# Kernel optimization log

Hardware: AMD Instinct MI355X
Metric: run time of the kernel (lower is better)

## Reference

```python
import jax, jax.numpy as jnp
import numpy as np

GAMMAS = (0.01, 0.1, 1.0, 10.0, 100.0)
FOCAL_GAMMA = 2.0
SMOOTH = 0.1
TASK_W = (0.4, 0.3, 0.3)
A_RECON, A_ORTH, A_ADV = 1.0, 0.1, 0.1
NUM_DOMAINS = 4
NUM_LABELS1 = 4


def focal_smooth(logits, targets, maskf):
    # FocalLoss.forward with smoothing > 0, masked mean
    n_classes = logits.shape[1]
    log_p = jax.nn.log_softmax(logits, axis=1)
    p = jnp.exp(log_p)
    onehot = jax.nn.one_hot(targets, n_classes, dtype=logits.dtype)
    smooth = onehot * (1.0 - SMOOTH) + SMOOTH / n_classes
    ce = -(smooth * log_p).sum(axis=1)
    pt = jnp.take_along_axis(p, targets[:, None], axis=1)[:, 0]
    loss = ce * (1.0 - pt) ** FOCAL_GAMMA
    return (loss * maskf).sum() / jnp.maximum(maskf.sum(), 1.0)


def ce_masked(logits, targets, maskf):
    log_p = jax.nn.log_softmax(logits, axis=1)
    nll = -jnp.take_along_axis(log_p, targets[:, None], axis=1)[:, 0]
    return (nll * maskf).sum() / jnp.maximum(maskf.sum(), 1.0)


def cond_mmd(feats, domains, labels, maskf):
    # Global pairwise sq-distance matrix; multi-gamma RBF kernels summed.
    sq = (feats ** 2).sum(axis=-1)                      # (B,)
    Dmat = sq[:, None] + sq[None, :] - 2.0 * feats @ feats.T  # (B,B)
    Ksum = jnp.zeros_like(Dmat)
    for g in GAMMAS:
        Ksum = Ksum + jnp.exp(-g * Dmat)
    loss = jnp.asarray(0.0, feats.dtype)
    count = jnp.asarray(0.0, feats.dtype)
    for lab in range(NUM_LABELS1):
        lm = (labels == lab).astype(feats.dtype) * maskf
        for d1 in range(NUM_DOMAINS):
            m1 = lm * (domains == d1).astype(feats.dtype)
            n1 = m1.sum()
            Km1 = Ksum @ m1
            for d2 in range(d1 + 1, NUM_DOMAINS):
                m2 = lm * (domains == d2).astype(feats.dtype)
                n2 = m2.sum()
                valid = (n1 > 1) & (n2 > 1)
                term = (m1 @ Km1) / jnp.maximum(n1, 1.0) ** 2 \
                     + (m2 @ (Ksum @ m2)) / jnp.maximum(n2, 1.0) ** 2 \
                     - 2.0 * (m2 @ Km1) / jnp.maximum(n1 * n2, 1.0)
                loss = loss + jnp.where(valid, term, 0.0)
                count = count + valid.astype(feats.dtype)
    return loss / jnp.maximum(count, 1.0)


def hsic(c, s):
    n = c.shape[0]
    c = c / jnp.maximum(jnp.linalg.norm(c, axis=-1, keepdims=True), 1e-12)
    s = s / jnp.maximum(jnp.linalg.norm(s, axis=-1, keepdims=True), 1e-12)
    K = c @ c.T
    L = s @ s.T
    Kc = K - K.mean(axis=0, keepdims=True) - K.mean(axis=1, keepdims=True) + K.mean()
    Lc = L - L.mean(axis=0, keepdims=True) - L.mean(axis=1, keepdims=True) + L.mean()
    return (Kc * Lc).sum() / (n - 1) ** 2


def setup_inputs() -> dict:
    key = jax.random.key(0)
    ks = jax.random.split(key, 20)
    B, D, H = 4096, 256, 768
    inp = {
        'logits1': jax.random.normal(ks[0], (B, 4), jnp.float32),
        'labels1': jax.random.randint(ks[1], (B,), 0, 4),
        'logits2': jax.random.normal(ks[2], (B, 6), jnp.float32),
        'labels2': jax.random.randint(ks[3], (B,), 0, 6),
        'logits3': jax.random.normal(ks[4], (B, 3), jnp.float32),
        'labels3': jax.random.randint(ks[5], (B,), 0, 3),
        'c_v': jax.random.normal(ks[6], (B, D), jnp.float32),
        's_v': jax.random.normal(ks[7], (B, D), jnp.float32),
        'c_t': jax.random.normal(ks[8], (B, D), jnp.float32),
        's_t': jax.random.normal(ks[9], (B, D), jnp.float32),
        'v_sv': jax.random.normal(ks[10], (B, NUM_DOMAINS), jnp.float32),
        'v_st': jax.random.normal(ks[11], (B, NUM_DOMAINS), jnp.float32),
        'domain_labels': jax.random.randint(ks[12], (B,), 0, NUM_DOMAINS),
        'mask': jnp.ones((B,), dtype=bool),
        'h_img_recon': jax.random.normal(ks[13], (B, H), jnp.float32),
        'h_img_orig': jax.random.normal(ks[14], (B, H), jnp.float32),
        'h_txt_recon': jax.random.normal(ks[15], (B, H), jnp.float32),
        'h_txt_orig': jax.random.normal(ks[16], (B, H), jnp.float32),
    }
    return inp


def reference(logits1, labels1, logits2, labels2, logits3, labels3,
              c_v, s_v, c_t, s_t, v_sv, v_st, domain_labels, mask,
              h_img_recon, h_img_orig, h_txt_recon, h_txt_orig):
    maskf = mask.astype(jnp.float32)
    total = jnp.asarray(0.0, jnp.float32)
    # classification (focal + label smoothing), per-task weighted
    total = total + TASK_W[0] * focal_smooth(logits1, labels1, maskf)
    total = total + TASK_W[1] * focal_smooth(logits2, labels2, maskf)
    total = total + TASK_W[2] * focal_smooth(logits3, labels3, maskf)
    # adversarial: CE on spurious domain logits + conditional MMD on causal feats
    l_adv_s = ce_masked(v_sv, domain_labels, maskf) + ce_masked(v_st, domain_labels, maskf)
    l_adv_c = cond_mmd(c_v, domain_labels, labels1, maskf) \
            + cond_mmd(c_t, domain_labels, labels1, maskf)
    total = total + A_ADV * (l_adv_s + l_adv_c)
    # orthogonality (HSIC), on unmasked features as in source
    l_orth = hsic(c_v, s_v) + hsic(c_t, s_t)
    total = total + A_ORTH * l_orth
    # reconstruction MSE
    l_recon = jnp.mean((h_img_recon - h_img_orig) ** 2) + jnp.mean((h_txt_recon - h_txt_orig) ** 2)
    total = total + A_RECON * l_recon
    return total
```

## Files before the change

### kernel.cpp

```cpp
#include <hip/hip_runtime.h>
#include <hip/hip_bf16.h>


typedef short bf16x8 __attribute__((ext_vector_type(8)));
typedef float f32x4 __attribute__((ext_vector_type(4)));
typedef unsigned long long u64;
typedef unsigned int u32;

static constexpr int D = 256;
static constexpr int H = 768;
static constexpr int NG = 16;
static constexpr float FX32 = 4294967296.f;
static constexpr float IFX32 = 2.3283064365386963e-10f;

__device__ inline void gAddFx(u64* p, float v) {
  long long q = (long long)llroundf(v * FX32);
  atomicAdd(p, (u64)q);
}
__device__ inline float fxToF(u64 v) { return (float)(long long)v * IFX32; }

__device__ inline float focal_n(const float* x, int n, int tgt,
                                float s_over_n, float oms) {
  float mx = x[0];
  for (int c = 1; c < n; ++c) mx = fmaxf(mx, x[c]);
  float se = 0.f, sx = 0.f;
  for (int c = 0; c < n; ++c) { se += __expf(x[c] - mx); sx += x[c]; }
  float logZ = mx + __logf(se);
  float ce = logZ - oms * x[tgt] - s_over_n * sx;
  float pt = __expf(x[tgt] - logZ);
  float om = 1.f - pt;
  return ce * om * om;
}

extern "C" __global__ __launch_bounds__(256) void k_pre(
    const void* __restrict__ mask, const int* __restrict__ y1,
    const int* __restrict__ dom,
    const float* __restrict__ l1, const float* __restrict__ l2,
    const float* __restrict__ l3, const int* __restrict__ y2,
    const int* __restrict__ y3,
    const float* __restrict__ vsv, const float* __restrict__ vst,
    const float* __restrict__ cv, const float* __restrict__ sv,
    const float* __restrict__ ct, const float* __restrict__ st,
    const float* __restrict__ ir, const float* __restrict__ io,
    const float* __restrict__ trc, const float* __restrict__ to,
    u64* SA, u64* GCU, u64* U64,
    int* gid, float* sq, float* inv, unsigned short* bf, u32* CNTB,
    int B, int N4, int NA, int NB) {
  __shared__ u32 sh3[3];
  __shared__ u32 cnt[17];
  __shared__ int redi[4];
  __shared__ float redf[4];
  int bid = blockIdx.x;
  int t = threadIdx.x;

  if (bid < NA) {
    if (t < 3) sh3[t] = 0;
    if (t < 17) cnt[t] = 0;
    __syncthreads();
    u32 a = 0, b2 = 0, cd = 0;
    if (t * 16 + 15 < B) {
      uint4 wv = ((const uint4*)mask)[t];
      u32 ws[4] = {wv.x, wv.y, wv.z, wv.w};
      #pragma unroll
      for (int j = 0; j < 4; ++j) {
        a |= ws[j] & 0xffu; b2 |= ws[j] & 0xff00u; cd |= ws[j] & 0xffff0000u;
      }
    }
    if (a) atomicOr(&sh3[0], 1u);
    if (b2) atomicOr(&sh3[1], 1u);
    if (cd) atomicOr(&sh3[2], 1u);
    __syncthreads();
    int mode;
    if ((sh3[1] | sh3[2]) == 0) mode = 0;
    else if (sh3[0] == 0 && sh3[1] == 0) mode = 1;
    else mode = 2;
    int r = bid * 256 + t;
    int mi = 0;
    float s[5] = {0.f, 0.f, 0.f, 0.f, 0.f};
    if (r < B) {
      if (mode == 0)      mi = ((const int*)mask)[r] ? 1 : 0;
      else if (mode == 1) mi = (((const float*)mask)[r] != 0.f) ? 1 : 0;
      else                mi = ((const unsigned char*)mask)[r] ? 1 : 0;
      int g = -1;
      if (mi) { g = y1[r] * 4 + dom[r]; atomicAdd(&cnt[g], 1u); }
      else atomicAdd(&cnt[16], 1u);
      gid[r] = g;
      if (mi) {
        float x[6];
        for (int c = 0; c < 4; ++c) x[c] = l1[r * 4 + c];
        s[0] = focal_n(x, 4, y1[r], 0.1f / 4.f, 0.9f);
        for (int c = 0; c < 6; ++c) x[c] = l2[r * 6 + c];
        s[1] = focal_n(x, 6, y2[r], 0.1f / 6.f, 0.9f);
        for (int c = 0; c < 3; ++c) x[c] = l3[r * 3 + c];
        s[2] = focal_n(x, 3, y3[r], 0.1f / 3.f, 0.9f);
        int d = dom[r];
        for (int c = 0; c < 4; ++c) x[c] = vsv[r * 4 + c];
        {
          float mx = fmaxf(fmaxf(x[0], x[1]), fmaxf(x[2], x[3]));
          float se = __expf(x[0]-mx)+__expf(x[1]-mx)+__expf(x[2]-mx)+__expf(x[3]-mx);
          s[3] = mx + __logf(se) - x[d];
        }
        for (int c = 0; c < 4; ++c) x[c] = vst[r * 4 + c];
        {
          float mx = fmaxf(fmaxf(x[0], x[1]), fmaxf(x[2], x[3]));
          float se = __expf(x[0]-mx)+__expf(x[1]-mx)+__expf(x[2]-mx)+__expf(x[3]-mx);
          s[4] = mx + __logf(se) - x[d];
        }
      }
    }
    int v = mi;
    #pragma unroll
    for (int o = 32; o > 0; o >>= 1) v += __shfl_down(v, o);
    if ((t & 63) == 0) redi[t >> 6] = v;
    __syncthreads();
    if (t == 0) atomicAdd(&SA[5], (u64)(redi[0] + redi[1] + redi[2] + redi[3]));
    if (t < NG && cnt[t]) atomicAdd(&GCU[t], (u64)cnt[t]);
    if (t < 17) CNTB[bid * 17 + t] = cnt[t];
    for (int k = 0; k < 5; ++k) {
      float x = s[k];
      #pragma unroll
      for (int o = 32; o > 0; o >>= 1) x += __shfl_down(x, o);
      __syncthreads();
      if ((t & 63) == 0) redf[t >> 6] = x;
      __syncthreads();
      if (t == 0) gAddFx(&SA[k], redf[0] + redf[1] + redf[2] + redf[3]);
    }
  } else if (bid < NA + NB) {
    int b = bid - NA;
    int f = b >> 6;
    int rb = b & 63;
    const float* p = (f == 0) ? cv : (f == 1) ? sv : (f == 2) ? ct : st;
    int w = t >> 6, L = t & 63;
    float up0 = 0.f, up1 = 0.f, up2 = 0.f, up3 = 0.f;
    for (int k = 0; k < 16; ++k) {
      int r = rb * 64 + w * 16 + k;
      float4 v = ((const float4*)(p + (size_t)r * D))[L];
      float ss = v.x * v.x + v.y * v.y + v.z * v.z + v.w * v.w;
      #pragma unroll
      for (int o = 32; o > 0; o >>= 1) ss += __shfl_down(ss, o);
      ss = __shfl(ss, 0);
      float iv = 1.f / fmaxf(sqrtf(ss), 1e-12f);
      if ((f & 1) == 0) {
        int fi = f >> 1;
        alignas(8) __hip_bfloat16 hb[4];
        hb[0] = __float2bfloat16(v.x); hb[1] = __float2bfloat16(v.y);
        hb[2] = __float2bfloat16(v.z); hb[3] = __float2bfloat16(v.w);
        *(uint2*)(bf + ((size_t)fi * B + r) * D + L * 4) = *(uint2*)hb;
        if (L == 0) sq[fi * B + r] = ss;
      }
      if (L == 0) inv[f * B + r] = iv;
      up0 += v.x * iv; up1 += v.y * iv; up2 += v.z * iv; up3 += v.w * iv;
    }
    u64* Uf = U64 + f * D + 4 * L;
    gAddFx(Uf + 0, up0); gAddFx(Uf + 1, up1);
    gAddFx(Uf + 2, up2); gAddFx(Uf + 3, up3);
  } else {
    int cidx = bid - (NA + NB);
    int j = cidx >> 8;
    int cb = cidx & 255;
    const float4* A  = (const float4*)(j ? trc : ir);
    const float4* Bp = (const float4*)(j ? to : io);
    float acc = 0.f;
    for (int idx = cb * 256 + t; idx < N4; idx += 256 * 256) {
      float4 a = A[idx], b = Bp[idx];
      float dx = a.x-b.x, dy = a.y-b.y, dz = a.z-b.z, dw = a.w-b.w;
      acc += dx*dx + dy*dy + dz*dz + dw*dw;
    }
    #pragma unroll
    for (int o = 32; o > 0; o >>= 1) acc += __shfl_down(acc, o);
    if ((t & 63) == 0) redf[t >> 6] = acc;
    __syncthreads();
    if (t == 0) gAddFx(&SA[6 + j], redf[0] + redf[1] + redf[2] + redf[3]);
  }
}

extern "C" __global__ __launch_bounds__(256) void k_mid(
    const u32* __restrict__ CNTB, const int* __restrict__ gid,
    const float* __restrict__ sq,
    const float* __restrict__ cv, const float* __restrict__ sv,
    const float* __restrict__ ct, const float* __restrict__ st,
    const float* __restrict__ inv,
    int* __restrict__ perm, float* __restrict__ sqp, int* __restrict__ OFF,
    unsigned short* __restrict__ bnT, int B, int NA) {
  __shared__ float ld[64 * 65];
  __shared__ u32 cbs[17], tots[17], wcnt[4][17];
  __shared__ u32 base[18];
  int b = blockIdx.x, t = threadIdx.x;

  if (b < NA) {
    if (t < 68) ((u32*)wcnt)[t] = 0;
    if (t < 17) {
      u32 cb = 0, tot = 0;
      for (int b2 = 0; b2 < NA; ++b2) {
        u32 c = CNTB[b2 * 17 + t];
        cb += (b2 < b) ? c : 0u;
        tot += c;
      }
      cbs[t] = cb; tots[t] = tot;
    }
    int r = b * 256 + t;
    int g = 16;
    if (r < B) { int gg = gid[r]; g = (gg < 0) ? 16 : gg; }
    __syncthreads();
    if (t == 0) {
      u32 s = 0;
      for (int g2 = 0; g2 < 17; ++g2) { base[g2] = s; s += tots[g2]; }
      base[17] = s;
    }
    u64 msk = ~0ull;
    #pragma unroll
    for (int bit = 0; bit < 5; ++bit) {
      int bv = (g >> bit) & 1;
      u64 bl = __ballot(bv);
      msk &= bv ? bl : ~bl;
    }
    int lane = t & 63, w = t >> 6;
    int rwave = __popcll(msk & ((1ull << lane) - 1ull));
    if (rwave == 0) wcnt[w][g] = (u32)__popcll(msk);
    __syncthreads();
    if (r < B) {
      int rank = rwave;
      for (int w2 = 0; w2 < 4; ++w2) if (w2 < w) rank += (int)wcnt[w2][g];
      int pos = (int)(base[g] + cbs[g]) + rank;
      perm[pos] = r;
      sqp[pos] = sq[r];
      sqp[B + pos] = sq[B + r];
    }
    if (b == 0 && t < 18) OFF[t] = (int)base[t];
  } else {
    int TPF = (B >> 6) * 4;
    int tb = b - NA;
    int fm = tb / TPF, tile = tb - fm * TPF;
    int it = tile >> 2, at = tile & 3;
    const float* src = (fm == 0) ? cv : (fm == 1) ? sv : (fm == 2) ? ct : st;
    const float* ivf = inv + (size_t)fm * B;
    int i0 = it * 64, a0 = at * 64;
    for (int e = t; e < 1024; e += 256) {
      int i = e >> 4, c4 = e & 15;
      float4 v = ((const float4*)(src + (size_t)(i0 + i) * D))[at * 16 + c4];
      float ivv = ivf[i0 + i];
      ld[i * 65 + c4 * 4 + 0] = v.x * ivv;
      ld[i * 65 + c4 * 4 + 1] = v.y * ivv;
      ld[i * 65 + c4 * 4 + 2] = v.z * ivv;
      ld[i * 65 + c4 * 4 + 3] = v.w * ivv;
    }
    __syncthreads();
    unsigned short* dst = bnT + (size_t)fm * D * B;
    for (int e = t; e < 512; e += 256) {
      int a = e >> 3, ic = e & 7;
      alignas(16) unsigned short h[8];
      #pragma unroll
      for (int j = 0; j < 8; ++j) {
        __hip_bfloat16 hb = __float2bfloat16(ld[(ic * 8 + j) * 65 + a]);
        h[j] = *(unsigned short*)&hb;
      }
      *(uint4*)(dst + (size_t)(a0 + a) * B + i0 + ic * 8) = *(uint4*)h;
    }
  }
}

extern "C" __global__ __launch_bounds__(256) void k_big(
    const unsigned short* __restrict__ bf, const float* __restrict__ sqp,
    const int* __restrict__ perm, const int* __restrict__ OFF,
    const unsigned short* __restrict__ bnT, float* __restrict__ Mf32,
    u64* GSP, int B) {
  __shared__ __align__(16) char smem[17536];
  unsigned short* Ab = (unsigned short*)smem;
  unsigned short* Bb = (unsigned short*)(smem + 8192);
  int bid = blockIdx.x;
  int tid = threadIdx.x;
  int w = tid >> 6, L = tid & 63, m = L & 15, q = L >> 4;
  int r0 = tid >> 3, ck = tid & 7;
  int swz = (ck ^ (r0 & 7)) * 8;
  int ar = w * 16 + m;

  if (bid < 64) {
    int half = bid & 1, bb = (bid >> 1) & 3, ab = (bid >> 3) & 3, p = (bid >> 5) & 1;
    const unsigned short* Abase = bnT + (size_t)(2 * p) * D * B;
    const unsigned short* Bbase = bnT + (size_t)(2 * p + 1) * D * B;
    size_t kof = (size_t)half * (B >> 1) + ck * 8;
    const uint4* gA0 = (const uint4*)(Abase + (size_t)(ab * 64 + r0) * B + kof);
    const uint4* gA1 = (const uint4*)(Abase + (size_t)(ab * 64 + r0 + 32) * B + kof);
    const uint4* gB0 = (const uint4*)(Bbase + (size_t)(bb * 64 + r0) * B + kof);
    const uint4* gB1 = (const uint4*)(Bbase + (size_t)(bb * 64 + r0 + 32) * B + kof);
    uint4* dA0 = (uint4*)&Ab[r0 * 64 + swz];
    uint4* dA1 = (uint4*)&Ab[(r0 + 32) * 64 + swz];
    uint4* dB0 = (uint4*)&Bb[r0 * 64 + swz];
    uint4* dB1 = (uint4*)&Bb[(r0 + 32) * 64 + swz];
    f32x4 acc[4] = {{0.f,0.f,0.f,0.f},{0.f,0.f,0.f,0.f},
                    {0.f,0.f,0.f,0.f},{0.f,0.f,0.f,0.f}};
    int nh = B >> 7;
    for (int hq = 0; hq < nh; ++hq) {
      *dA0 = gA0[hq * 8]; *dA1 = gA1[hq * 8];
      *dB0 = gB0[hq * 8]; *dB1 = gB1[hq * 8];
      __syncthreads();
      #pragma unroll
      for (int kk = 0; kk < 2; ++kk) {
        bf16x8 aF = *(const bf16x8*)&Ab[ar * 64 + (((kk * 4 + q) ^ (ar & 7)) * 8)];
        #pragma unroll
        for (int c = 0; c < 4; ++c) {
          int br = c * 16 + m;
          bf16x8 bF = *(const bf16x8*)&Bb[br * 64 + (((kk * 4 + q) ^ (br & 7)) * 8)];
          acc[c] = __builtin_amdgcn_mfma_f32_16x16x32_bf16(aF, bF, acc[c], 0, 0, 0);
        }
      }
      if (hq < nh - 1) __syncthreads();
    }
    float* Mo = Mf32 + (size_t)(half * 2 + p) * D * D;
    int ri0 = w * 16 + q * 4;
    #pragma unroll
    for (int c = 0; c < 4; ++c) {
      #pragma unroll
      for (int v = 0; v < 4; ++v)
        Mo[(size_t)(ab * 64 + ri0 + v) * D + bb * 64 + c * 16 + m] = acc[c][v];
    }
    return;
  }

  float* sA = (float*)(smem + 16384);
  float* sB = (float*)(smem + 16640);
  int*   pA = (int*)(smem + 16896);
  int*   pB = (int*)(smem + 17152);
  int*   offs = (int*)(smem + 17408);

  int idx2 = bid - 64;
  int feat = idx2 & 1;
  int tlin = idx2 >> 1;
  int NT = B / 64;
  float tf = (float)tlin;
  int ti = (int)((2.f * NT + 1.f -
                  sqrtf((2.f * NT + 1.f) * (2.f * NT + 1.f) - 8.f * tf)) * 0.5f);
  while (ti > 0 && (ti * NT - (ti * (ti - 1)) / 2) > tlin) --ti;
  while (((ti + 1) * NT - ((ti + 1) * ti) / 2) <= tlin) ++ti;
  int tj = ti + (tlin - (ti * NT - (ti * (ti - 1)) / 2));
  int i0 = ti * 64, j0 = tj * 64;
  bool diag = (ti == tj);
  const unsigned short* fb = bf + (size_t)feat * B * D;
  const float* sqf = sqp + (size_t)feat * B;

  if (tid < 64) { pA[tid] = perm[i0 + tid]; sA[tid] = sqf[i0 + tid]; }
  else if (tid < 128) { int r = tid - 64; pB[r] = perm[j0 + r]; sB[r] = sqf[j0 + r]; }
  else if (tid < 146) offs[tid - 128] = OFF[tid - 128];
  __syncthreads();

  int gr0 = 0, nbr = 0, gc0 = 0, ncb = 0;
  #pragma unroll
  for (int g = 1; g <= 17; ++g) {
    int o = offs[g];
    gr0 += (o <= i0) ? 1 : 0;
    nbr += (o > i0 && o < i0 + 64) ? 1 : 0;
    gc0 += (o <= j0) ? 1 : 0;
    ncb += (o > j0 && o < j0 + 64) ? 1 : 0;
  }
  if (gr0 == 16 || gc0 == 16) return;
  int gr1 = gr0 + nbr;
  int gc1 = gc0 + ncb;
  int s_r = nbr ? offs[gr1] : i0 + 64;
  int s_c = ncb ? offs[gc1] : j0 + 64;

  const uint4* gA0 = (const uint4*)(fb + (size_t)pA[r0] * D + ck * 8);
  const uint4* gA1 = (const uint4*)(fb + (size_t)pA[r0 + 32] * D + ck * 8);
  uint4* dA0 = (uint4*)&Ab[r0 * 64 + swz];
  uint4* dA1 = (uint4*)&Ab[(r0 + 32) * 64 + swz];
  const uint4* gB0 = nullptr; const uint4* gB1 = nullptr;
  uint4* dB0 = nullptr; uint4* dB1 = nullptr;
  if (!diag) {
    gB0 = (const uint4*)(fb + (size_t)pB[r0] * D + ck * 8);
    gB1 = (const uint4*)(fb + (size_t)pB[r0 + 32] * D + ck * 8);
    dB0 = (uint4*)&Bb[r0 * 64 + swz];
    dB1 = (uint4*)&Bb[(r0 + 32) * 64 + swz];
  }
  const unsigned short* Bp = diag ? Ab : Bb;

  f32x4 acc[4] = {{0.f,0.f,0.f,0.f},{0.f,0.f,0.f,0.f},
                  {0.f,0.f,0.f,0.f},{0.f,0.f,0.f,0.f}};

  for (int hq = 0; hq < 4; ++hq) {
    *dA0 = gA0[hq * 8]; *dA1 = gA1[hq * 8];
    if (!diag) { *dB0 = gB0[hq * 8]; *dB1 = gB1[hq * 8]; }
    __syncthreads();
    #pragma unroll
    for (int kk = 0; kk < 2; ++kk) {
      bf16x8 aF = *(const bf16x8*)&Ab[ar * 64 + (((kk * 4 + q) ^ (ar & 7)) * 8)];
      #pragma unroll
      for (int c = 0; c < 4; ++c) {
        int br = c * 16 + m;
        bf16x8 bF = *(const bf16x8*)&Bp[br * 64 + (((kk * 4 + q) ^ (br & 7)) * 8)];
        acc[c] = __builtin_amdgcn_mfma_f32_16x16x32_bf16(aF, bF, acc[c], 0, 0, 0);
      }
    }
    if (hq < 3) __syncthreads();
  }

  int ri0 = w * 16 + q * 4;
  u64* gsp = GSP + ((size_t)(tlin & 63) * 2 + feat) * NG * NG;

  if (nbr <= 1 && ncb <= 1) {
    float siv[4]; bool rhiv[4];
    #pragma unroll
    for (int v = 0; v < 4; ++v) {
      siv[v] = sA[ri0 + v];
      rhiv[v] = (i0 + ri0 + v) >= s_r;
    }
    float a00 = 0.f, a01 = 0.f, a10 = 0.f, a11 = 0.f;
    #pragma unroll
    for (int c = 0; c < 4; ++c) {
      int rj = c * 16 + m;
      float sb = sB[rj];
      float lo = 0.f, hi = 0.f;
      #pragma unroll
      for (int v = 0; v < 4; ++v) {
        float d = fmaxf(siv[v] + sb - 2.f * acc[c][v], 0.f);
        float K = __expf(-0.01f * d) + __expf(-0.1f * d) + __expf(-d)
                + __expf(-10.f * d) + __expf(-100.f * d);
        if (diag) {
          int ri = ri0 + v;
          K = (ri > rj) ? 0.f : (ri == rj) ? 5.f : K;
        }
        float kh = rhiv[v] ? K : 0.f;
        hi += kh; lo += K - kh;
      }
      bool chi = (j0 + rj) >= s_c;
      float loH = chi ? lo : 0.f;
      float hiH = chi ? hi : 0.f;
      a00 += lo - loH; a01 += loH;
      a10 += hi - hiH; a11 += hiH;
    }
    #pragma unroll
    for (int o = 32; o > 0; o >>= 1) {
      a00 += __shfl_down(a00, o); a01 += __shfl_down(a01, o);
      a10 += __shfl_down(a10, o); a11 += __shfl_down(a11, o);
    }
    if (L == 0) {
      if (a00 != 0.f)
        atomicAdd(&gsp[gr0 * NG + gc0], (u64)(long long)llroundf(a00 * 65536.f));
      if (a01 != 0.f && gc1 < 16)
        atomicAdd(&gsp[gr0 * NG + gc1], (u64)(long long)llroundf(a01 * 65536.f));
      if (a10 != 0.f && gr1 < 16)
        atomicAdd(&gsp[gr1 * NG + gc0], (u64)(long long)llroundf(a10 * 65536.f));
      if (a11 != 0.f && gr1 < 16 && gc1 < 16)
        atomicAdd(&gsp[gr1 * NG + gc1], (u64)(long long)llroundf(a11 * 65536.f));
    }
  } else {
    int giv[4]; float siv[4];
    #pragma unroll
    for (int v = 0; v < 4; ++v) {
      int idx = i0 + ri0 + v;
      int g = 0;
      #pragma unroll
      for (int k = 1; k <= 16; ++k) g += (offs[k] <= idx) ? 1 : 0;
      giv[v] = g;
      siv[v] = sA[ri0 + v];
    }
    #pragma unroll
    for (int c = 0; c < 4; ++c) {
      int rj = c * 16 + m;
      int jdx = j0 + rj;
      int gj = 0;
      #pragma unroll
      for (int k = 1; k <= 16; ++k) gj += (offs[k] <= jdx) ? 1 : 0;
      float sb = sB[rj];
      #pragma unroll
      for (int v = 0; v < 4; ++v) {
        int ri = ri0 + v;
        if (giv[v] < 16 && gj < 16 && !(diag && ri > rj)) {
          float K;
          if (diag && ri == rj) K = 5.f;
          else {
            float d = fmaxf(siv[v] + sb - 2.f * acc[c][v], 0.f);
            K = __expf(-0.01f * d) + __expf(-0.1f * d) + __expf(-d)
              + __expf(-10.f * d) + __expf(-100.f * d);
          }
          u32 kf = (u32)(K * 65536.f + 0.5f);
          atomicAdd(&gsp[giv[v] * NG + gj], (u64)kf);
        }
      }
    }
  }
}

extern "C" __global__ __launch_bounds__(256) void k_hsic(
    const u64* __restrict__ U64, const float* __restrict__ Mf32, u64* SA) {
  __shared__ float red[8];
  __shared__ float ush[32], vsh[D];
  int p = blockIdx.y;
  int k0 = blockIdx.x * 32;
  int t = threadIdx.x;
  vsh[t] = fxToF(U64[(2 * p + 1) * D + t]);
  if (t < 32) ush[t] = fxToF(U64[(2 * p) * D + k0 + t]);
  __syncthreads();
  const float* M0 = Mf32 + (size_t)p * D * D;
  const float* M1 = Mf32 + (size_t)(2 + p) * D * D;
  float trkl = 0.f, cr = 0.f;
  #pragma unroll 4
  for (int k = 0; k < 32; ++k) {
    float mv = M0[(size_t)(k0 + k) * D + t] + M1[(size_t)(k0 + k) * D + t];
    trkl += mv * mv;
    cr += ush[k] * mv;
  }
  cr *= vsh[t];
  #pragma unroll
  for (int o = 32; o > 0; o >>= 1) { trkl += __shfl_down(trkl, o); cr += __shfl_down(cr, o); }
  if ((t & 63) == 0) { red[t >> 6] = trkl; red[4 + (t >> 6)] = cr; }
  __syncthreads();
  if (t == 0) gAddFx(&SA[10 + p], red[0] + red[1] + red[2] + red[3]);
  if (t == 64) gAddFx(&SA[12 + p], red[4] + red[5] + red[6] + red[7]);
}

extern "C" __global__ __launch_bounds__(256) void k_final(
    const u64* SA, const u64* GCU, const u64* GSP,
    const u64* U64, float* out, int B) {
  __shared__ float red[8];
  __shared__ float gssh[2 * NG * NG];
  int t = threadIdx.x;
  for (int e = t; e < 2 * NG * NG; e += 256) {
    u64 ssum = 0;
    int f = e >> 8, idx = e & 255;
    for (int cpy = 0; cpy < 64; ++cpy)
      ssum += GSP[((size_t)cpy * 2 + f) * NG * NG + idx];
    gssh[e] = (float)((double)ssum * (1.0 / 65536.0));
  }
  __syncthreads();

  float n = (float)B;
  float hs[2];
  for (int p = 0; p < 2; ++p) {
    float ut = fxToF(U64[(2 * p) * D + t]);
    float vt = fxToF(U64[(2 * p + 1) * D + t]);
    float uu = ut * ut, vv = vt * vt;
    #pragma unroll
    for (int o = 32; o > 0; o >>= 1) { uu += __shfl_down(uu, o); vv += __shfl_down(vv, o); }
    __syncthreads();
    if ((t & 63) == 0) { red[t >> 6] = uu; red[4 + (t >> 6)] = vv; }
    __syncthreads();
    float uus = red[0] + red[1] + red[2] + red[3];
    float vvs = red[4] + red[5] + red[6] + red[7];
    float trkl = (float)((double)(long long)SA[10 + p] * (double)IFX32);
    float cr   = (float)((double)(long long)SA[12 + p] * (double)IFX32);
    hs[p] = (trkl - (2.f / n) * cr + uus * vvs / (n * n))
          / ((n - 1.f) * (n - 1.f));
    __syncthreads();
  }
  if (t == 0) {
    float msum = fmaxf((float)SA[5], 1.f);
    float f1 = fxToF(SA[0]) / msum;
    float f2 = fxToF(SA[1]) / msum;
    float f3 = fxToF(SA[2]) / msum;
    float cesv = fxToF(SA[3]) / msum;
    float cest = fxToF(SA[4]) / msum;
    float mmd[2];
    for (int f = 0; f < 2; ++f) {
      float loss = 0.f, cntv = 0.f;
      for (int lab = 0; lab < 4; ++lab)
        for (int d1 = 0; d1 < 4; ++d1)
          for (int d2 = d1 + 1; d2 < 4; ++d2) {
            int a = lab * 4 + d1, b = lab * 4 + d2;
            float n1 = (float)GCU[a], n2 = (float)GCU[b];
            if (n1 > 1.f && n2 > 1.f) {
              float g11 = 2.f * gssh[f * 256 + a * NG + a] - 5.f * n1;
              float g22 = 2.f * gssh[f * 256 + b * NG + b] - 5.f * n2;
              float g12 = gssh[f * 256 + a * NG + b];
              loss += g11 / (fmaxf(n1, 1.f) * fmaxf(n1, 1.f))
                    + g22 / (fmaxf(n2, 1.f) * fmaxf(n2, 1.f))
                    - 2.f * g12 / fmaxf(n1 * n2, 1.f);
              cntv += 1.f;
            }
          }
      mmd[f] = loss / fmaxf(cntv, 1.f);
    }
    double rs = ((double)(long long)SA[6] + (double)(long long)SA[7])
              * (double)IFX32;
    float recon = (float)(rs / ((double)B * (double)H));
    float total = 0.4f * f1 + 0.3f * f2 + 0.3f * f3
                + 0.1f * (cesv + cest + mmd[0] + mmd[1])
                + 0.1f * (hs[0] + hs[1])
                + recon;
    out[0] = total;
  }
}

extern "C" void kernel_launch(void* const* d_in, const int* in_sizes, int n_in,
                              void* d_out, int out_size, void* d_ws, size_t ws_size,
                              hipStream_t stream) {
  const float* l1  = (const float*)d_in[0];
  const int*   y1  = (const int*)d_in[1];
  const float* l2  = (const float*)d_in[2];
  const int*   y2  = (const int*)d_in[3];
  const float* l3  = (const float*)d_in[4];
  const int*   y3  = (const int*)d_in[5];
  const float* cv  = (const float*)d_in[6];
  const float* sv  = (const float*)d_in[7];
  const float* ct  = (const float*)d_in[8];
  const float* st  = (const float*)d_in[9];
  const float* vsv = (const float*)d_in[10];
  const float* vst = (const float*)d_in[11];
  const int*   dom = (const int*)d_in[12];
  const void*  mask= d_in[13];
  const float* ir  = (const float*)d_in[14];
  const float* io  = (const float*)d_in[15];
  const float* trc = (const float*)d_in[16];
  const float* to  = (const float*)d_in[17];
  int B = in_sizes[1];

  u64* SA  = (u64*)d_ws;
  u64* GCU = SA + 32;
  u64* U64 = GCU + 16;
  u64* GSP = U64 + 4 * D;
  u64* zend = GSP + 64 * 2 * NG * NG;
  size_t zeroBytes = (size_t)((char*)zend - (char*)d_ws);
  unsigned short* bf  = (unsigned short*)zend;
  unsigned short* bnT = bf + 2 * (size_t)B * D;
  float* Mf32 = (float*)(bnT + 4 * (size_t)D * B);
  int*   gid = (int*)(Mf32 + 4 * (size_t)D * D);
  float* sq  = (float*)(gid + B);
  float* inv = sq + 2 * B;
  int*   perm = (int*)(inv + 4 * B);
  float* sqp  = (float*)(perm + B);
  int*   OFF  = (int*)(sqp + 2 * B);
  u32*   CNTB = (u32*)(OFF + 18);

  int NA = B / 256;
  int NB = 4 * (B / 64);
  int NC = 512;
  int N4 = B * H / 4;

  hipMemsetAsync(d_ws, 0, zeroBytes, stream);
  k_pre<<<NA + NB + NC, 256, 0, stream>>>(
      mask, y1, dom, l1, l2, l3, y2, y3, vsv, vst,
      cv, sv, ct, st, ir, io, trc, to,
      SA, GCU, U64, gid, sq, inv, bf, CNTB, B, N4, NA, NB);
  int NTR = B / 4;
  k_mid<<<NA + NTR, 256, 0, stream>>>(CNTB, gid, sq, cv, sv, ct, st, inv,
                                      perm, sqp, OFF, bnT, B, NA);
  int NT = B / 64;
  int nmmd = 2 * (NT * (NT + 1) / 2);
  k_big<<<64 + nmmd, 256, 0, stream>>>(bf, sqp, perm, OFF, bnT, Mf32, GSP, B);
  k_hsic<<<dim3(8, 2), 256, 0, stream>>>(U64, Mf32, SA);
  k_final<<<1, 256, 0, stream>>>(SA, GCU, GSP, U64, (float*)d_out, B);
}
```

Measured before the change: 222.3 us.

## Rebalance k_pre work: more norm blocks, chunked recon reduction, batched shuffles

Restructures k_pre's three roles. The loss-sum reduction now folds five serial reduce/sync rounds into one shuffle pass with a single barrier. The norm blocks handle 32 rows instead of 64, with batched loads and shuffles, and combine per-wave U partials in shared memory before one set of atomics. The reconstruction-MSE section doubles its block count to 1024, uses contiguous chunks and a 2x unrolled loop. The aim is more parallelism and memory-level concurrency plus fewer global atomics, at the cost of more blocks and extra shared memory per block.

New measurement: 207.9 us. 1.07x faster.

```diff
diff --git a/kernel.cpp b/kernel.cpp
--- a/kernel.cpp
+++ b/kernel.cpp
@@ -50,6 +50,8 @@
   __shared__ u32 cnt[17];
   __shared__ int redi[4];
   __shared__ float redf[4];
+  __shared__ float redf5[5][4];
+  __shared__ float ub[4][64][4];
   int bid = blockIdx.x;
   int t = threadIdx.x;
 
@@ -110,58 +112,98 @@
     }
     int v = mi;
     #pragma unroll
-    for (int o = 32; o > 0; o >>= 1) v += __shfl_down(v, o);
-    if ((t & 63) == 0) redi[t >> 6] = v;
-    __syncthreads();
-    if (t == 0) atomicAdd(&SA[5], (u64)(redi[0] + redi[1] + redi[2] + redi[3]));
+    for (int o = 32; o > 0; o >>= 1) {
+      v += __shfl_down(v, o);
+      #pragma unroll
+      for (int k = 0; k < 5; ++k) s[k] += __shfl_down(s[k], o);
+    }
+    if ((t & 63) == 0) {
+      redi[t >> 6] = v;
+      #pragma unroll
+      for (int k = 0; k < 5; ++k) redf5[k][t >> 6] = s[k];
+    }
+    __syncthreads();
+    if (t == 0) {
+      atomicAdd(&SA[5], (u64)(redi[0] + redi[1] + redi[2] + redi[3]));
+      #pragma unroll
+      for (int k = 0; k < 5; ++k)
+        gAddFx(&SA[k], redf5[k][0] + redf5[k][1] + redf5[k][2] + redf5[k][3]);
+    }
     if (t < NG && cnt[t]) atomicAdd(&GCU[t], (u64)cnt[t]);
     if (t < 17) CNTB[bid * 17 + t] = cnt[t];
-    for (int k = 0; k < 5; ++k) {
-      float x = s[k];
-      #pragma unroll
-      for (int o = 32; o > 0; o >>= 1) x += __shfl_down(x, o);
-      __syncthreads();
-      if ((t & 63) == 0) redf[t >> 6] = x;
-      __syncthreads();
-      if (t == 0) gAddFx(&SA[k], redf[0] + redf[1] + redf[2] + redf[3]);
-    }
   } else if (bid < NA + NB) {
     int b = bid - NA;
-    int f = b >> 6;
-    int rb = b & 63;
+    int perF = NB >> 2;
+    int f = b / perF;
+    int rb = b - f * perF;
     const float* p = (f == 0) ? cv : (f == 1) ? sv : (f == 2) ? ct : st;
     int w = t >> 6, L = t & 63;
     float up0 = 0.f, up1 = 0.f, up2 = 0.f, up3 = 0.f;
-    for (int k = 0; k < 16; ++k) {
-      int r = rb * 64 + w * 16 + k;
-      float4 v = ((const float4*)(p + (size_t)r * D))[L];
-      float ss = v.x * v.x + v.y * v.y + v.z * v.z + v.w * v.w;
-      #pragma unroll
-      for (int o = 32; o > 0; o >>= 1) ss += __shfl_down(ss, o);
-      ss = __shfl(ss, 0);
-      float iv = 1.f / fmaxf(sqrtf(ss), 1e-12f);
-      if ((f & 1) == 0) {
-        int fi = f >> 1;
-        alignas(8) __hip_bfloat16 hb[4];
-        hb[0] = __float2bfloat16(v.x); hb[1] = __float2bfloat16(v.y);
-        hb[2] = __float2bfloat16(v.z); hb[3] = __float2bfloat16(v.w);
-        *(uint2*)(bf + ((size_t)fi * B + r) * D + L * 4) = *(uint2*)hb;
-        if (L == 0) sq[fi * B + r] = ss;
-      }
-      if (L == 0) inv[f * B + r] = iv;
-      up0 += v.x * iv; up1 += v.y * iv; up2 += v.z * iv; up3 += v.w * iv;
-    }
-    u64* Uf = U64 + f * D + 4 * L;
-    gAddFx(Uf + 0, up0); gAddFx(Uf + 1, up1);
-    gAddFx(Uf + 2, up2); gAddFx(Uf + 3, up3);
+    for (int bt = 0; bt < 2; ++bt) {
+      int rbase = rb * 32 + w * 8 + bt * 4;
+      float4 vv[4];
+      #pragma unroll
+      for (int i = 0; i < 4; ++i)
+        vv[i] = ((const float4*)(p + (size_t)(rbase + i) * D))[L];
+      float ss[4];
+      #pragma unroll
+      for (int i = 0; i < 4; ++i)
+        ss[i] = vv[i].x * vv[i].x + vv[i].y * vv[i].y
+              + vv[i].z * vv[i].z + vv[i].w * vv[i].w;
+      #pragma unroll
+      for (int o = 32; o > 0; o >>= 1) {
+        #pragma unroll
+        for (int i = 0; i < 4; ++i) ss[i] += __shfl_down(ss[i], o);
+      }
+      #pragma unroll
+      for (int i = 0; i < 4; ++i) ss[i] = __shfl(ss[i], 0);
+      #pragma unroll
+      for (int i = 0; i < 4; ++i) {
+        int r = rbase + i;
+        float iv = 1.f / fmaxf(sqrtf(ss[i]), 1e-12f);
+        if ((f & 1) == 0) {
+          int fi = f >> 1;
+          alignas(8) __hip_bfloat16 hb[4];
+          hb[0] = __float2bfloat16(vv[i].x); hb[1] = __float2bfloat16(vv[i].y);
+          hb[2] = __float2bfloat16(vv[i].z); hb[3] = __float2bfloat16(vv[i].w);
+          *(uint2*)(bf + ((size_t)fi * B + r) * D + L * 4) = *(uint2*)hb;
+          if (L == 0) sq[fi * B + r] = ss[i];
+        }
+        if (L == 0) inv[f * B + r] = iv;
+        up0 += vv[i].x * iv; up1 += vv[i].y * iv;
+        up2 += vv[i].z * iv; up3 += vv[i].w * iv;
+      }
+    }
+    ub[w][L][0] = up0; ub[w][L][1] = up1; ub[w][L][2] = up2; ub[w][L][3] = up3;
+    __syncthreads();
+    if (t < 64) {
+      u64* Uf = U64 + f * D + 4 * t;
+      #pragma unroll
+      for (int j = 0; j < 4; ++j) {
+        float s4 = ub[0][t][j] + ub[1][t][j] + ub[2][t][j] + ub[3][t][j];
+        gAddFx(Uf + j, s4);
+      }
+    }
   } else {
     int cidx = bid - (NA + NB);
-    int j = cidx >> 8;
-    int cb = cidx & 255;
+    int j = cidx >> 9;
+    int cb = cidx & 511;
     const float4* A  = (const float4*)(j ? trc : ir);
     const float4* Bp = (const float4*)(j ? to : io);
+    int CH = (N4 + 511) >> 9;
+    int base = cb * CH;
+    int end = min(base + CH, N4);
     float acc = 0.f;
-    for (int idx = cb * 256 + t; idx < N4; idx += 256 * 256) {
+    int idx = base + t;
+    for (; idx + 256 < end; idx += 512) {
+      float4 a0 = A[idx],       b0 = Bp[idx];
+      float4 a1 = A[idx + 256], b1 = Bp[idx + 256];
+      float dx0 = a0.x-b0.x, dy0 = a0.y-b0.y, dz0 = a0.z-b0.z, dw0 = a0.w-b0.w;
+      float dx1 = a1.x-b1.x, dy1 = a1.y-b1.y, dz1 = a1.z-b1.z, dw1 = a1.w-b1.w;
+      acc += dx0*dx0 + dy0*dy0 + dz0*dz0 + dw0*dw0
+           + dx1*dx1 + dy1*dy1 + dz1*dz1 + dw1*dw1;
+    }
+    if (idx < end) {
       float4 a = A[idx], b = Bp[idx];
       float dx = a.x-b.x, dy = a.y-b.y, dz = a.z-b.z, dw = a.w-b.w;
       acc += dx*dx + dy*dy + dz*dz + dw*dw;
@@ -620,8 +662,8 @@
   u32*   CNTB = (u32*)(OFF + 18);
 
   int NA = B / 256;
-  int NB = 4 * (B / 64);
-  int NC = 512;
+  int NB = B / 8;
+  int NC = 1024;
   int N4 = B * H / 4;
 
   hipMemsetAsync(d_ws, 0, zeroBytes, stream);
```
